# Kernel tuning notes

Hardware: AMD Instinct MI355X
Metric: run time of the kernel (lower is better)

Reference implementation:

```python
import jax, jax.numpy as jnp
import numpy as np

B, S, D = 2, 4096, 1024
H = 16
HD = D // H  # 64


def setup_inputs() -> dict:
    key = jax.random.key(0)
    ks = jax.random.split(key, 5)
    scale = 1.0 / np.sqrt(D)
    return {
        "x": jax.random.normal(ks[0], (B, S, D), dtype=jnp.float32),
        "Wq": jax.random.normal(ks[1], (D, D), dtype=jnp.float32) * scale,
        "Wk": jax.random.normal(ks[2], (D, D), dtype=jnp.float32) * scale,
        "Wv": jax.random.normal(ks[3], (D, D), dtype=jnp.float32) * scale,
        "Wo": jax.random.normal(ks[4], (D, D), dtype=jnp.float32) * scale,
        "bo": jnp.zeros((D,), dtype=jnp.float32),
    }


def reference(x, Wq, Wk, Wv, Wo, bo):
    b, s, d = x.shape
    # Linear layers (torch layout: weight [out, in], y = x @ W.T)
    q = (x @ Wq.T).reshape(b, s, H, HD)
    k = (x @ Wk.T).reshape(b, s, H, HD)
    v = (x @ Wv.T).reshape(b, s, H, HD)
    # scores: [b, h, q, k]
    scores = jnp.einsum("bqhd,bkhd->bhqk", q, k)
    # causal mask (upper triangle above diagonal -> -inf)
    causal = jnp.triu(jnp.ones((s, s), dtype=bool), k=1)
    scores = jnp.where(causal[None, None], -jnp.inf, scores)
    weights = jax.nn.softmax(scores / np.sqrt(HD), axis=-1)  # dropout p=0.0 -> identity
    ctx = jnp.einsum("bhqk,bkhd->bqhd", weights, v).reshape(b, s, d)
    return ctx @ Wo.T + bo
```

## Files before the change

kernel.cpp:

```cpp
#include <hip/hip_runtime.h>
#include <stdint.h>
#include <stddef.h>

#define S_LEN 4096
#define NHEAD 16
#define HDIM 64
#define DMODEL 1024
#define NBATCH 2
#define LOG2E 1.4426950408889634f

typedef __attribute__((ext_vector_type(8))) short bf16x8;
typedef __attribute__((ext_vector_type(4))) float f32x4;
typedef __attribute__((ext_vector_type(16))) float f32x16;
typedef __attribute__((ext_vector_type(2))) unsigned int uint2v;
typedef __attribute__((ext_vector_type(4))) unsigned int uint4v;

__device__ inline unsigned short f2b(float f) {
    union { float f; unsigned int u; } x; x.f = f;
    unsigned int r = (x.u + 0x7fffu + ((x.u >> 16) & 1u)) >> 16;
    return (unsigned short)r;
}

__device__ inline unsigned cvt_pk_bf16(float lo, float hi) {
    unsigned r;
    asm("v_cvt_pk_bf16_f32 %0, %1, %2" : "=v"(r) : "v"(lo), "v"(hi));
    return r;
}

__device__ inline float exp_fast(float x) {
    float r;
    asm("v_exp_f32 %0, %1" : "=v"(r) : "v"(x));
    return r;
}

__device__ inline void gload_lds16(const void* g, void* l) {
    __builtin_amdgcn_global_load_lds((const __attribute__((address_space(1))) void*)g,
                                     (__attribute__((address_space(3))) void*)l,
                                     16, 0, 0);
}

__global__ void cvt_x(const float* __restrict__ in, unsigned short* __restrict__ out, int n4) {
    int i = blockIdx.x * 256 + threadIdx.x;
    if (i >= n4) return;
    float4 v = ((const float4*)in)[i];
    ushort4 o;
    o.x = f2b(v.x); o.y = f2b(v.y); o.z = f2b(v.z); o.w = f2b(v.w);
    ((ushort4*)out)[i] = o;
}

__global__ void cvt_w(const float* __restrict__ w0, const float* __restrict__ w1,
                      const float* __restrict__ w2, const float* __restrict__ w3,
                      unsigned short* __restrict__ dst) {
    int z = blockIdx.y;
    const float* src = (z == 0) ? w0 : (z == 1) ? w1 : (z == 2) ? w2 : w3;
    int i = blockIdx.x * 256 + threadIdx.x;
    float4 v = ((const float4*)src)[i];
    ushort4 o;
    o.x = f2b(v.x); o.y = f2b(v.y); o.z = f2b(v.z); o.w = f2b(v.w);
    ((ushort4*)(dst + (size_t)z * DMODEL * DMODEL))[i] = o;
}

__global__ __launch_bounds__(256, 2)
void gemm_qkv(const unsigned short* __restrict__ xb,
              const unsigned short* __restrict__ wqb,
              const unsigned short* __restrict__ wkb,
              const unsigned short* __restrict__ wvb,
              unsigned short* __restrict__ Qb,
              unsigned short* __restrict__ Kb,
              unsigned short* __restrict__ Vt,
              float qscale) {
    __shared__ unsigned short Asl[128 * 64];
    __shared__ unsigned short Bsl[128 * 64];
    const int tid  = threadIdx.x;
    const int lane = tid & 63;
    const int wid  = tid >> 6;
    const int wm   = (wid >> 1) * 64, wn = (wid & 1) * 64;
    const int lr   = lane & 15, lk = lane >> 4;
    const int z    = blockIdx.z;

    const unsigned short* A;
    const unsigned short* Bw;
    int m0, n0;
    if (z < 2) { A = xb; Bw = z ? wkb : wqb; m0 = blockIdx.x * 128; n0 = blockIdx.y * 128; }
    else       { A = wvb; Bw = xb;           m0 = blockIdx.y * 128; n0 = blockIdx.x * 128; }

    f32x4 acc[4][4];
#pragma unroll
    for (int i = 0; i < 4; ++i)
#pragma unroll
        for (int j = 0; j < 4; ++j) acc[i][j] = (f32x4){0.f, 0.f, 0.f, 0.f};

    for (int kt = 0; kt < DMODEL; kt += 64) {
#pragma unroll
        for (int i = 0; i < 4; ++i) {
            int c = i * 256 + tid;
            int r = c >> 3, gc = (c & 7) ^ (r & 7);
            gload_lds16(A + (size_t)(m0 + r) * DMODEL + kt + gc * 8, Asl + c * 8);
        }
#pragma unroll
        for (int i = 0; i < 4; ++i) {
            int c = i * 256 + tid;
            int r = c >> 3, gc = (c & 7) ^ (r & 7);
            gload_lds16(Bw + (size_t)(n0 + r) * DMODEL + kt + gc * 8, Bsl + c * 8);
        }
        __syncthreads();
#pragma unroll
        for (int kh = 0; kh < 2; ++kh) {
            int cl = kh * 4 + lk;
            bf16x8 af[4], bfr[4];
#pragma unroll
            for (int m = 0; m < 4; ++m) {
                int r = wm + m * 16 + lr;
                af[m] = *(const bf16x8*)(Asl + r * 64 + ((cl ^ (r & 7)) * 8));
            }
#pragma unroll
            for (int n = 0; n < 4; ++n) {
                int r = wn + n * 16 + lr;
                bfr[n] = *(const bf16x8*)(Bsl + r * 64 + ((cl ^ (r & 7)) * 8));
            }
#pragma unroll
            for (int m = 0; m < 4; ++m)
#pragma unroll
                for (int n = 0; n < 4; ++n)
                    acc[m][n] = __builtin_amdgcn_mfma_f32_16x16x32_bf16(af[m], bfr[n], acc[m][n], 0, 0, 0);
        }
        __syncthreads();
    }

#pragma unroll
    for (int m = 0; m < 4; ++m) {
#pragma unroll
        for (int n = 0; n < 4; ++n) {
            int gn = n0 + wn + n * 16 + lr;
#pragma unroll
            for (int r = 0; r < 4; ++r) {
                int gm = m0 + wm + m * 16 + lk * 4 + r;
                float v = acc[m][n][r];
                if (z == 0) {
                    int b = gm >> 12, s = gm & 4095, h = gn >> 6, hd = gn & 63;
                    Qb[((size_t)((b * NHEAD + h) * S_LEN + s)) * HDIM + hd] = f2b(v * qscale);
                } else if (z == 1) {
                    int b = gm >> 12, s = gm & 4095, h = gn >> 6, hd = gn & 63;
                    Kb[((size_t)((b * NHEAD + h) * S_LEN + s)) * HDIM + hd] = f2b(v);
                } else {
                    int h = gm >> 6, hd = gm & 63, b = gn >> 12, s = gn & 4095;
                    Vt[((size_t)((b * NHEAD + h) * HDIM + hd)) * S_LEN + s] = f2b(v);
                }
            }
        }
    }
}

__global__ __launch_bounds__(256, 2)
void gemm_out(const unsigned short* __restrict__ A,
              const unsigned short* __restrict__ Bw,
              float* __restrict__ out, const float* __restrict__ bias) {
    __shared__ unsigned short Asl[128 * 64];
    __shared__ unsigned short Bsl[128 * 64];
    const int tid  = threadIdx.x;
    const int lane = tid & 63;
    const int wid  = tid >> 6;
    const int wm   = (wid >> 1) * 64, wn = (wid & 1) * 64;
    const int lr   = lane & 15, lk = lane >> 4;
    const int m0   = blockIdx.x * 128, n0 = blockIdx.y * 128;

    f32x4 acc[4][4];
#pragma unroll
    for (int i = 0; i < 4; ++i)
#pragma unroll
        for (int j = 0; j < 4; ++j) acc[i][j] = (f32x4){0.f, 0.f, 0.f, 0.f};

    for (int kt = 0; kt < DMODEL; kt += 64) {
#pragma unroll
        for (int i = 0; i < 4; ++i) {
            int c = i * 256 + tid;
            int r = c >> 3, gc = (c & 7) ^ (r & 7);
            gload_lds16(A + (size_t)(m0 + r) * DMODEL + kt + gc * 8, Asl + c * 8);
        }
#pragma unroll
        for (int i = 0; i < 4; ++i) {
            int c = i * 256 + tid;
            int r = c >> 3, gc = (c & 7) ^ (r & 7);
            gload_lds16(Bw + (size_t)(n0 + r) * DMODEL + kt + gc * 8, Bsl + c * 8);
        }
        __syncthreads();
#pragma unroll
        for (int kh = 0; kh < 2; ++kh) {
            int cl = kh * 4 + lk;
            bf16x8 af[4], bfr[4];
#pragma unroll
            for (int m = 0; m < 4; ++m) {
                int r = wm + m * 16 + lr;
                af[m] = *(const bf16x8*)(Asl + r * 64 + ((cl ^ (r & 7)) * 8));
            }
#pragma unroll
            for (int n = 0; n < 4; ++n) {
                int r = wn + n * 16 + lr;
                bfr[n] = *(const bf16x8*)(Bsl + r * 64 + ((cl ^ (r & 7)) * 8));
            }
#pragma unroll
            for (int m = 0; m < 4; ++m)
#pragma unroll
                for (int n = 0; n < 4; ++n)
                    acc[m][n] = __builtin_amdgcn_mfma_f32_16x16x32_bf16(af[m], bfr[n], acc[m][n], 0, 0, 0);
        }
        __syncthreads();
    }
#pragma unroll
    for (int m = 0; m < 4; ++m)
#pragma unroll
        for (int n = 0; n < 4; ++n) {
            int gn = n0 + wn + n * 16 + lr;
#pragma unroll
            for (int r = 0; r < 4; ++r) {
                int gm = m0 + wm + m * 16 + lk * 4 + r;
                out[(size_t)gm * DMODEL + gn] = acc[m][n][r] + bias[gn];
            }
        }
}

__global__ __launch_bounds__(256)
void attn_fwd(const unsigned short* __restrict__ Q,
              const unsigned short* __restrict__ K,
              const unsigned short* __restrict__ Vt,
              unsigned short* __restrict__ ctx) {
    __shared__ unsigned short Kl[2][4096];
    __shared__ unsigned short Vl[2][4096];

    const int tid  = threadIdx.x;
    const int lane = tid & 63;
    const int w    = tid >> 6;
    const int l31  = lane & 31;
    const int hi   = lane >> 5;

    const int bid  = blockIdx.x;
    const int qt   = 31 - (bid >> 5);
    const int bh   = ((bid & 7) << 2) | ((bid >> 3) & 3);
    const int b    = bh >> 4, h = bh & 15;
    const int q0   = qt * 128;
    const int qw0  = q0 + w * 32;

    const unsigned short* Qh = Q  + (size_t)bh * S_LEN * HDIM;
    const unsigned short* Kh = K  + (size_t)bh * S_LEN * HDIM;
    const unsigned short* Vh = Vt + (size_t)bh * HDIM * S_LEN;

    const int skA  = tid >> 6;
    const int lS   = tid & 63;
    const int lS31 = lS & 31, hiS = lS >> 5;
    const unsigned short* kb0 = Kh + (size_t)lS31 * HDIM + skA * 16 + hiS * 8;
    const unsigned short* kb1 = Kh + (size_t)(32 + lS31) * HDIM + skA * 16 + hiS * 8;
    const unsigned short* vb0 = Vh + (size_t)lS31 * S_LEN + skA * 16 + hiS * 8;
    const unsigned short* vb1 = Vh + (size_t)(32 + lS31) * S_LEN + skA * 16 + hiS * 8;

    bf16x8 qf[4];
    {
        const unsigned short* qrow = Qh + (size_t)(qw0 + l31) * HDIM + hi * 8;
#pragma unroll
        for (int s = 0; s < 4; ++s) qf[s] = *(const bf16x8*)(qrow + s * 16);
    }

    bf16x8 ones;
#pragma unroll
    for (int j = 0; j < 8; ++j) ones[j] = (short)0x3F80;

    f32x16 z16;
#pragma unroll
    for (int j = 0; j < 16; ++j) z16[j] = 0.f;

    const unsigned short* KL = &Kl[0][0] + lane * 8;
    const unsigned short* VL = &Vl[0][0] + lane * 8;

    f32x16 o0, o1, ls;
#pragma unroll
    for (int j = 0; j < 16; ++j) { o0[j] = 0.f; o1[j] = 0.f; ls[j] = 0.f; }

    const int nt = 2 * qt + 2;

    auto stage = [&](int buf, int kv0) {
        gload_lds16(kb0 + (size_t)kv0 * HDIM, &Kl[buf][(size_t)tid * 8]);
        gload_lds16(kb1 + (size_t)kv0 * HDIM, &Kl[buf][2048 + (size_t)tid * 8]);
        gload_lds16(vb0 + kv0, &Vl[buf][(size_t)tid * 8]);
        gload_lds16(vb1 + kv0, &Vl[buf][2048 + (size_t)tid * 8]);
    };

    auto packfrag = [&](const f32x16& v, int base) -> bf16x8 {
        unsigned a0 = cvt_pk_bf16(v[base + 0], v[base + 1]), a1 = cvt_pk_bf16(v[base + 2], v[base + 3]);
        unsigned b0 = cvt_pk_bf16(v[base + 4], v[base + 5]), b1 = cvt_pk_bf16(v[base + 6], v[base + 7]);
        uint2v r0 = __builtin_amdgcn_permlane32_swap(a0, b0, false, false);
        uint2v r1 = __builtin_amdgcn_permlane32_swap(a1, b1, false, false);
        uint4v f; f.x = r0.x; f.y = r1.x; f.z = r0.y; f.w = r1.y;
        return __builtin_bit_cast(bf16x8, f);
    };

    auto compute = [&](int buf, int kv0) {
        const unsigned short* KB = KL + buf * 4096;
        const unsigned short* VB = VL + buf * 4096;
        const int q = qw0 + l31;

        if (kv0 < qw0 + 32) {
            __builtin_amdgcn_s_setprio(1);
            f32x16 st = __builtin_amdgcn_mfma_f32_32x32x16_bf16(
                            *(const bf16x8*)(KB + 0 * 512), qf[0], z16, 0, 0, 0);
#pragma unroll
            for (int s = 1; s < 4; ++s)
                st = __builtin_amdgcn_mfma_f32_32x32x16_bf16(
                        *(const bf16x8*)(KB + s * 512), qf[s], st, 0, 0, 0);
            __builtin_amdgcn_s_setprio(0);
            if (kv0 + 31 > qw0) {
#pragma unroll
                for (int j = 0; j < 16; ++j) {
                    int roff = (j & 3) + 8 * (j >> 2) + 4 * hi;
                    if (kv0 + roff > q) st[j] = -3e38f;
                }
            }
#pragma unroll
            for (int j = 0; j < 16; ++j) st[j] = exp_fast(st[j]);
            bf16x8 pa = packfrag(st, 0);
            bf16x8 pb = packfrag(st, 8);
            __builtin_amdgcn_s_setprio(1);
            ls = __builtin_amdgcn_mfma_f32_32x32x16_bf16(ones, pa, ls, 0, 0, 0);
            ls = __builtin_amdgcn_mfma_f32_32x32x16_bf16(ones, pb, ls, 0, 0, 0);
            o0 = __builtin_amdgcn_mfma_f32_32x32x16_bf16(*(const bf16x8*)(VB + 0 * 512), pa, o0, 0, 0, 0);
            o1 = __builtin_amdgcn_mfma_f32_32x32x16_bf16(*(const bf16x8*)(VB + 4 * 512), pa, o1, 0, 0, 0);
            o0 = __builtin_amdgcn_mfma_f32_32x32x16_bf16(*(const bf16x8*)(VB + 1 * 512), pb, o0, 0, 0, 0);
            o1 = __builtin_amdgcn_mfma_f32_32x32x16_bf16(*(const bf16x8*)(VB + 5 * 512), pb, o1, 0, 0, 0);
            __builtin_amdgcn_s_setprio(0);
        }

        if (kv0 < qw0) {
            __builtin_amdgcn_s_setprio(1);
            f32x16 st = __builtin_amdgcn_mfma_f32_32x32x16_bf16(
                            *(const bf16x8*)(KB + 4 * 512), qf[0], z16, 0, 0, 0);
#pragma unroll
            for (int s = 1; s < 4; ++s)
                st = __builtin_amdgcn_mfma_f32_32x32x16_bf16(
                        *(const bf16x8*)(KB + (4 + s) * 512), qf[s], st, 0, 0, 0);
            __builtin_amdgcn_s_setprio(0);
            if (kv0 + 63 > qw0) {
#pragma unroll
                for (int j = 0; j < 16; ++j) {
                    int roff = (j & 3) + 8 * (j >> 2) + 4 * hi;
                    if (kv0 + 32 + roff > q) st[j] = -3e38f;
                }
            }
#pragma unroll
            for (int j = 0; j < 16; ++j) st[j] = exp_fast(st[j]);
            bf16x8 pa = packfrag(st, 0);
            bf16x8 pb = packfrag(st, 8);
            __builtin_amdgcn_s_setprio(1);
            ls = __builtin_amdgcn_mfma_f32_32x32x16_bf16(ones, pa, ls, 0, 0, 0);
            ls = __builtin_amdgcn_mfma_f32_32x32x16_bf16(ones, pb, ls, 0, 0, 0);
            o0 = __builtin_amdgcn_mfma_f32_32x32x16_bf16(*(const bf16x8*)(VB + 2 * 512), pa, o0, 0, 0, 0);
            o1 = __builtin_amdgcn_mfma_f32_32x32x16_bf16(*(const bf16x8*)(VB + 6 * 512), pa, o1, 0, 0, 0);
            o0 = __builtin_amdgcn_mfma_f32_32x32x16_bf16(*(const bf16x8*)(VB + 3 * 512), pb, o0, 0, 0, 0);
            o1 = __builtin_amdgcn_mfma_f32_32x32x16_bf16(*(const bf16x8*)(VB + 7 * 512), pb, o1, 0, 0, 0);
            __builtin_amdgcn_s_setprio(0);
        }
    };

    stage(0, 0);
    __syncthreads();
    for (int t = 0; t < nt; t += 2) {
        const int kv0 = t * 64;
        stage(1, kv0 + 64);
        compute(0, kv0);
        __syncthreads();
        if (t + 2 < nt) stage(0, kv0 + 128);
        compute(1, kv0 + 64);
        __syncthreads();
    }

    float inv = 1.f / ls[0];
    size_t sq = (size_t)q0 + w * 32 + l31;
    unsigned short* crow = ctx + ((size_t)b * S_LEN + sq) * DMODEL + h * HDIM;
#pragma unroll
    for (int quad = 0; quad < 4; ++quad) {
        int hdbase = quad * 8 + hi * 4;
        unsigned w0 = cvt_pk_bf16(o0[4 * quad] * inv, o0[4 * quad + 1] * inv);
        unsigned w1 = cvt_pk_bf16(o0[4 * quad + 2] * inv, o0[4 * quad + 3] * inv);
        *(unsigned long long*)(crow + hdbase) = ((unsigned long long)w1 << 32) | w0;
        unsigned w2 = cvt_pk_bf16(o1[4 * quad] * inv, o1[4 * quad + 1] * inv);
        unsigned w3 = cvt_pk_bf16(o1[4 * quad + 2] * inv, o1[4 * quad + 3] * inv);
        *(unsigned long long*)(crow + 32 + hdbase) = ((unsigned long long)w3 << 32) | w2;
    }
}

extern "C" void kernel_launch(void* const* d_in, const int* in_sizes, int n_in,
                              void* d_out, int out_size, void* d_ws, size_t ws_size,
                              hipStream_t stream) {
    (void)in_sizes; (void)n_in; (void)out_size; (void)ws_size;
    const float* x  = (const float*)d_in[0];
    const float* Wq = (const float*)d_in[1];
    const float* Wk = (const float*)d_in[2];
    const float* Wv = (const float*)d_in[3];
    const float* Wo = (const float*)d_in[4];
    const float* bo = (const float*)d_in[5];

    unsigned short* ws  = (unsigned short*)d_ws;
    const size_t NTOK = (size_t)NBATCH * S_LEN;
    unsigned short* xb  = ws;
    unsigned short* wqb = xb  + NTOK * DMODEL;
    unsigned short* wkb = wqb + (size_t)DMODEL * DMODEL;
    unsigned short* wvb = wkb + (size_t)DMODEL * DMODEL;
    unsigned short* wob = wvb + (size_t)DMODEL * DMODEL;
    unsigned short* Qb  = wob + (size_t)DMODEL * DMODEL;
    unsigned short* Kb  = Qb  + NTOK * DMODEL;
    unsigned short* Vt  = Kb  + NTOK * DMODEL;
    unsigned short* ctx = xb;

    int n4x = (int)(NTOK * DMODEL / 4);
    cvt_x<<<(n4x + 255) / 256, 256, 0, stream>>>(x, xb, n4x);
    cvt_w<<<dim3(DMODEL * DMODEL / 4 / 256, 4), 256, 0, stream>>>(Wq, Wk, Wv, Wo, wqb);

    const float qscale = 0.125f * LOG2E;
    gemm_qkv<<<dim3(64, 8, 3), 256, 0, stream>>>(xb, wqb, wkb, wvb, Qb, Kb, Vt, qscale);

    attn_fwd<<<1024, 256, 0, stream>>>(Qb, Kb, Vt, ctx);

    gemm_out<<<dim3(64, 8), 256, 0, stream>>>(ctx, wob, (float*)d_out, bo);
}
```

Measured before the change: 193.5 us.

## Double query rows per wave in attention to reuse K/V tiles

Each wave now handles two 32-row query sub-tiles (256 queries per block) instead of one, so every K fragment and V tile loaded from LDS feeds two query groups, halving LDS reads and K/V global staging per query. The grid shrinks from 1024 to 512 blocks, and blocks are reordered with heaviest tiles first to balance the causal workload. The change adds register pressure (two sets of accumulators and Q fragments), constrained by launch_bounds(256,2), and gives fewer blocks for load balancing across CUs.

```diff
diff --git a/kernel.cpp b/kernel.cpp
--- a/kernel.cpp
+++ b/kernel.cpp
@@ -219,7 +219,7 @@
         }
 }
 
-__global__ __launch_bounds__(256)
+__global__ __launch_bounds__(256, 2)
 void attn_fwd(const unsigned short* __restrict__ Q,
               const unsigned short* __restrict__ K,
               const unsigned short* __restrict__ Vt,
@@ -234,11 +234,13 @@
     const int hi   = lane >> 5;
 
     const int bid  = blockIdx.x;
-    const int qt   = 31 - (bid >> 5);
+    const int g    = bid >> 5;
+    const int qt   = (g < 8) ? (15 - g) : (g - 8);
     const int bh   = ((bid & 7) << 2) | ((bid >> 3) & 3);
     const int b    = bh >> 4, h = bh & 15;
-    const int q0   = qt * 128;
-    const int qw0  = q0 + w * 32;
+    const int q0   = qt * 256;
+    const int qA   = q0 + w * 64;
+    const int qB   = qA + 32;
 
     const unsigned short* Qh = Q  + (size_t)bh * S_LEN * HDIM;
     const unsigned short* Kh = K  + (size_t)bh * S_LEN * HDIM;
@@ -252,11 +254,12 @@
     const unsigned short* vb0 = Vh + (size_t)lS31 * S_LEN + skA * 16 + hiS * 8;
     const unsigned short* vb1 = Vh + (size_t)(32 + lS31) * S_LEN + skA * 16 + hiS * 8;
 
-    bf16x8 qf[4];
-    {
-        const unsigned short* qrow = Qh + (size_t)(qw0 + l31) * HDIM + hi * 8;
-#pragma unroll
-        for (int s = 0; s < 4; ++s) qf[s] = *(const bf16x8*)(qrow + s * 16);
+    bf16x8 qf[2][4];
+#pragma unroll
+    for (int qs = 0; qs < 2; ++qs) {
+        const unsigned short* qrow = Qh + (size_t)(qA + qs * 32 + l31) * HDIM + hi * 8;
+#pragma unroll
+        for (int s = 0; s < 4; ++s) qf[qs][s] = *(const bf16x8*)(qrow + s * 16);
     }
 
     bf16x8 ones;
@@ -270,11 +273,13 @@
     const unsigned short* KL = &Kl[0][0] + lane * 8;
     const unsigned short* VL = &Vl[0][0] + lane * 8;
 
-    f32x16 o0, o1, ls;
-#pragma unroll
-    for (int j = 0; j < 16; ++j) { o0[j] = 0.f; o1[j] = 0.f; ls[j] = 0.f; }
-
-    const int nt = 2 * qt + 2;
+    f32x16 o0[2], o1[2], ls[2];
+#pragma unroll
+    for (int qs = 0; qs < 2; ++qs)
+#pragma unroll
+        for (int j = 0; j < 16; ++j) { o0[qs][j] = 0.f; o1[qs][j] = 0.f; ls[qs][j] = 0.f; }
+
+    const int nt = 4 * qt + 4;
 
     auto stage = [&](int buf, int kv0) {
         gload_lds16(kb0 + (size_t)kv0 * HDIM, &Kl[buf][(size_t)tid * 8]);
@@ -295,66 +300,46 @@
     auto compute = [&](int buf, int kv0) {
         const unsigned short* KB = KL + buf * 4096;
         const unsigned short* VB = VL + buf * 4096;
-        const int q = qw0 + l31;
-
-        if (kv0 < qw0 + 32) {
-            __builtin_amdgcn_s_setprio(1);
-            f32x16 st = __builtin_amdgcn_mfma_f32_32x32x16_bf16(
-                            *(const bf16x8*)(KB + 0 * 512), qf[0], z16, 0, 0, 0);
-#pragma unroll
-            for (int s = 1; s < 4; ++s)
-                st = __builtin_amdgcn_mfma_f32_32x32x16_bf16(
-                        *(const bf16x8*)(KB + s * 512), qf[s], st, 0, 0, 0);
-            __builtin_amdgcn_s_setprio(0);
-            if (kv0 + 31 > qw0) {
-#pragma unroll
-                for (int j = 0; j < 16; ++j) {
-                    int roff = (j & 3) + 8 * (j >> 2) + 4 * hi;
-                    if (kv0 + roff > q) st[j] = -3e38f;
+#pragma unroll
+        for (int half = 0; half < 2; ++half) {
+            const int kvh = kv0 + 32 * half;
+            if (kvh >= qB + 32) continue;
+            bf16x8 kf0 = *(const bf16x8*)(KB + (4 * half + 0) * 512);
+            bf16x8 kf1 = *(const bf16x8*)(KB + (4 * half + 1) * 512);
+            bf16x8 kf2 = *(const bf16x8*)(KB + (4 * half + 2) * 512);
+            bf16x8 kf3 = *(const bf16x8*)(KB + (4 * half + 3) * 512);
+#pragma unroll
+            for (int qs = 0; qs < 2; ++qs) {
+                const int qw = qA + qs * 32;
+                if (kvh < qw + 32) {
+                    __builtin_amdgcn_s_setprio(1);
+                    f32x16 st = __builtin_amdgcn_mfma_f32_32x32x16_bf16(kf0, qf[qs][0], z16, 0, 0, 0);
+                    st = __builtin_amdgcn_mfma_f32_32x32x16_bf16(kf1, qf[qs][1], st, 0, 0, 0);
+                    st = __builtin_amdgcn_mfma_f32_32x32x16_bf16(kf2, qf[qs][2], st, 0, 0, 0);
+                    st = __builtin_amdgcn_mfma_f32_32x32x16_bf16(kf3, qf[qs][3], st, 0, 0, 0);
+                    __builtin_amdgcn_s_setprio(0);
+                    if (kvh + 31 > qw) {
+                        const int q = qw + l31;
+#pragma unroll
+                        for (int j = 0; j < 16; ++j) {
+                            int roff = (j & 3) + 8 * (j >> 2) + 4 * hi;
+                            if (kvh + roff > q) st[j] = -3e38f;
+                        }
+                    }
+#pragma unroll
+                    for (int j = 0; j < 16; ++j) st[j] = exp_fast(st[j]);
+                    bf16x8 pa = packfrag(st, 0);
+                    bf16x8 pb = packfrag(st, 8);
+                    __builtin_amdgcn_s_setprio(1);
+                    ls[qs] = __builtin_amdgcn_mfma_f32_32x32x16_bf16(ones, pa, ls[qs], 0, 0, 0);
+                    ls[qs] = __builtin_amdgcn_mfma_f32_32x32x16_bf16(ones, pb, ls[qs], 0, 0, 0);
+                    o0[qs] = __builtin_amdgcn_mfma_f32_32x32x16_bf16(*(const bf16x8*)(VB + (2 * half + 0) * 512), pa, o0[qs], 0, 0, 0);
+                    o1[qs] = __builtin_amdgcn_mfma_f32_32x32x16_bf16(*(const bf16x8*)(VB + (2 * half + 4) * 512), pa, o1[qs], 0, 0, 0);
+                    o0[qs] = __builtin_amdgcn_mfma_f32_32x32x16_bf16(*(const bf16x8*)(VB + (2 * half + 1) * 512), pb, o0[qs], 0, 0, 0);
+                    o1[qs] = __builtin_amdgcn_mfma_f32_32x32x16_bf16(*(const bf16x8*)(VB + (2 * half + 5) * 512), pb, o1[qs], 0, 0, 0);
+                    __builtin_amdgcn_s_setprio(0);
                 }
             }
-#pragma unroll
-            for (int j = 0; j < 16; ++j) st[j] = exp_fast(st[j]);
-            bf16x8 pa = packfrag(st, 0);
-            bf16x8 pb = packfrag(st, 8);
-            __builtin_amdgcn_s_setprio(1);
-            ls = __builtin_amdgcn_mfma_f32_32x32x16_bf16(ones, pa, ls, 0, 0, 0);
-            ls = __builtin_amdgcn_mfma_f32_32x32x16_bf16(ones, pb, ls, 0, 0, 0);
-            o0 = __builtin_amdgcn_mfma_f32_32x32x16_bf16(*(const bf16x8*)(VB + 0 * 512), pa, o0, 0, 0, 0);
-            o1 = __builtin_amdgcn_mfma_f32_32x32x16_bf16(*(const bf16x8*)(VB + 4 * 512), pa, o1, 0, 0, 0);
-            o0 = __builtin_amdgcn_mfma_f32_32x32x16_bf16(*(const bf16x8*)(VB + 1 * 512), pb, o0, 0, 0, 0);
-            o1 = __builtin_amdgcn_mfma_f32_32x32x16_bf16(*(const bf16x8*)(VB + 5 * 512), pb, o1, 0, 0, 0);
-            __builtin_amdgcn_s_setprio(0);
-        }
-
-        if (kv0 < qw0) {
-            __builtin_amdgcn_s_setprio(1);
-            f32x16 st = __builtin_amdgcn_mfma_f32_32x32x16_bf16(
-                            *(const bf16x8*)(KB + 4 * 512), qf[0], z16, 0, 0, 0);
-#pragma unroll
-            for (int s = 1; s < 4; ++s)
-                st = __builtin_amdgcn_mfma_f32_32x32x16_bf16(
-                        *(const bf16x8*)(KB + (4 + s) * 512), qf[s], st, 0, 0, 0);
-            __builtin_amdgcn_s_setprio(0);
-            if (kv0 + 63 > qw0) {
-#pragma unroll
-                for (int j = 0; j < 16; ++j) {
-                    int roff = (j & 3) + 8 * (j >> 2) + 4 * hi;
-                    if (kv0 + 32 + roff > q) st[j] = -3e38f;
-                }
-            }
-#pragma unroll
-            for (int j = 0; j < 16; ++j) st[j] = exp_fast(st[j]);
-            bf16x8 pa = packfrag(st, 0);
-            bf16x8 pb = packfrag(st, 8);
-            __builtin_amdgcn_s_setprio(1);
-            ls = __builtin_amdgcn_mfma_f32_32x32x16_bf16(ones, pa, ls, 0, 0, 0);
-            ls = __builtin_amdgcn_mfma_f32_32x32x16_bf16(ones, pb, ls, 0, 0, 0);
-            o0 = __builtin_amdgcn_mfma_f32_32x32x16_bf16(*(const bf16x8*)(VB + 2 * 512), pa, o0, 0, 0, 0);
-            o1 = __builtin_amdgcn_mfma_f32_32x32x16_bf16(*(const bf16x8*)(VB + 6 * 512), pa, o1, 0, 0, 0);
-            o0 = __builtin_amdgcn_mfma_f32_32x32x16_bf16(*(const bf16x8*)(VB + 3 * 512), pb, o0, 0, 0, 0);
-            o1 = __builtin_amdgcn_mfma_f32_32x32x16_bf16(*(const bf16x8*)(VB + 7 * 512), pb, o1, 0, 0, 0);
-            __builtin_amdgcn_s_setprio(0);
         }
     };
 
@@ -370,18 +355,21 @@
         __syncthreads();
     }
 
-    float inv = 1.f / ls[0];
-    size_t sq = (size_t)q0 + w * 32 + l31;
-    unsigned short* crow = ctx + ((size_t)b * S_LEN + sq) * DMODEL + h * HDIM;
-#pragma unroll
-    for (int quad = 0; quad < 4; ++quad) {
-        int hdbase = quad * 8 + hi * 4;
-        unsigned w0 = cvt_pk_bf16(o0[4 * quad] * inv, o0[4 * quad + 1] * inv);
-        unsigned w1 = cvt_pk_bf16(o0[4 * quad + 2] * inv, o0[4 * quad + 3] * inv);
-        *(unsigned long long*)(crow + hdbase) = ((unsigned long long)w1 << 32) | w0;
-        unsigned w2 = cvt_pk_bf16(o1[4 * quad] * inv, o1[4 * quad + 1] * inv);
-        unsigned w3 = cvt_pk_bf16(o1[4 * quad + 2] * inv, o1[4 * quad + 3] * inv);
-        *(unsigned long long*)(crow + 32 + hdbase) = ((unsigned long long)w3 << 32) | w2;
+#pragma unroll
+    for (int qs = 0; qs < 2; ++qs) {
+        float inv = 1.f / ls[qs][0];
+        size_t sq = (size_t)qA + qs * 32 + l31;
+        unsigned short* crow = ctx + ((size_t)b * S_LEN + sq) * DMODEL + h * HDIM;
+#pragma unroll
+        for (int quad = 0; quad < 4; ++quad) {
+            int hdbase = quad * 8 + hi * 4;
+            unsigned w0 = cvt_pk_bf16(o0[qs][4 * quad] * inv, o0[qs][4 * quad + 1] * inv);
+            unsigned w1 = cvt_pk_bf16(o0[qs][4 * quad + 2] * inv, o0[qs][4 * quad + 3] * inv);
+            *(unsigned long long*)(crow + hdbase) = ((unsigned long long)w1 << 32) | w0;
+            unsigned w2 = cvt_pk_bf16(o1[qs][4 * quad] * inv, o1[qs][4 * quad + 1] * inv);
+            unsigned w3 = cvt_pk_bf16(o1[qs][4 * quad + 2] * inv, o1[qs][4 * quad + 3] * inv);
+            *(unsigned long long*)(crow + 32 + hdbase) = ((unsigned long long)w3 << 32) | w2;
+        }
     }
 }
 
@@ -415,7 +403,7 @@
     const float qscale = 0.125f * LOG2E;
     gemm_qkv<<<dim3(64, 8, 3), 256, 0, stream>>>(xb, wqb, wkb, wvb, Qb, Kb, Vt, qscale);
 
-    attn_fwd<<<1024, 256, 0, stream>>>(Qb, Kb, Vt, ctx);
+    attn_fwd<<<512, 256, 0, stream>>>(Qb, Kb, Vt, ctx);
 
     gemm_out<<<dim3(64, 8), 256, 0, stream>>>(ctx, wob, (float*)d_out, bo);
 }
```

After: 204.0 us. 1.05x slower.

## Use 4-deep 32-row KV ring buffer with partial vmcnt waits in attention

Applied to the files above, without the earlier changes.

Restructures the attention KV loop from a 2-buffer, 64-row ping-pong with full __syncthreads into a 4-slot ring of 32-row tiles. Three tiles are prefetched ahead, and each step waits only on the oldest loads with s_waitcnt vmcnt plus a raw s_barrier. The goal is to keep more global-to-LDS loads in flight and avoid draining all outstanding memory before every compute step. In exchange there are twice as many barriers per KV row, and correctness depends on the hand-written vmcnt counts matching the loads in flight.

```diff
diff --git a/kernel.cpp b/kernel.cpp
--- a/kernel.cpp
+++ b/kernel.cpp
@@ -224,8 +224,8 @@
               const unsigned short* __restrict__ K,
               const unsigned short* __restrict__ Vt,
               unsigned short* __restrict__ ctx) {
-    __shared__ unsigned short Kl[2][4096];
-    __shared__ unsigned short Vl[2][4096];
+    __shared__ unsigned short Kl[4][2048];
+    __shared__ unsigned short Vl[4][2048];
 
     const int tid  = threadIdx.x;
     const int lane = tid & 63;
@@ -244,13 +244,11 @@
     const unsigned short* Kh = K  + (size_t)bh * S_LEN * HDIM;
     const unsigned short* Vh = Vt + (size_t)bh * HDIM * S_LEN;
 
-    const int skA  = tid >> 6;
+    const int sk   = tid >> 6;
     const int lS   = tid & 63;
     const int lS31 = lS & 31, hiS = lS >> 5;
-    const unsigned short* kb0 = Kh + (size_t)lS31 * HDIM + skA * 16 + hiS * 8;
-    const unsigned short* kb1 = Kh + (size_t)(32 + lS31) * HDIM + skA * 16 + hiS * 8;
-    const unsigned short* vb0 = Vh + (size_t)lS31 * S_LEN + skA * 16 + hiS * 8;
-    const unsigned short* vb1 = Vh + (size_t)(32 + lS31) * S_LEN + skA * 16 + hiS * 8;
+    const unsigned short* kbase = Kh + (size_t)lS31 * HDIM + sk * 16 + hiS * 8;
+    const unsigned short* vbase = Vh + (size_t)((sk >> 1) * 32 + lS31) * S_LEN + (sk & 1) * 16 + hiS * 8;
 
     bf16x8 qf[4];
     {
@@ -274,13 +272,11 @@
 #pragma unroll
     for (int j = 0; j < 16; ++j) { o0[j] = 0.f; o1[j] = 0.f; ls[j] = 0.f; }
 
-    const int nt = 2 * qt + 2;
-
-    auto stage = [&](int buf, int kv0) {
-        gload_lds16(kb0 + (size_t)kv0 * HDIM, &Kl[buf][(size_t)tid * 8]);
-        gload_lds16(kb1 + (size_t)kv0 * HDIM, &Kl[buf][2048 + (size_t)tid * 8]);
-        gload_lds16(vb0 + kv0, &Vl[buf][(size_t)tid * 8]);
-        gload_lds16(vb1 + kv0, &Vl[buf][2048 + (size_t)tid * 8]);
+    const int nt = 4 * qt + 4;
+
+    auto stage = [&](int buf, int t) {
+        gload_lds16(kbase + (size_t)(t * 32) * HDIM, &Kl[buf][(size_t)tid * 8]);
+        gload_lds16(vbase + t * 32, &Vl[buf][(size_t)tid * 8]);
     };
 
     auto packfrag = [&](const f32x16& v, int base) -> bf16x8 {
@@ -293,82 +289,51 @@
     };
 
     auto compute = [&](int buf, int kv0) {
-        const unsigned short* KB = KL + buf * 4096;
-        const unsigned short* VB = VL + buf * 4096;
-        const int q = qw0 + l31;
-
-        if (kv0 < qw0 + 32) {
-            __builtin_amdgcn_s_setprio(1);
-            f32x16 st = __builtin_amdgcn_mfma_f32_32x32x16_bf16(
-                            *(const bf16x8*)(KB + 0 * 512), qf[0], z16, 0, 0, 0);
-#pragma unroll
-            for (int s = 1; s < 4; ++s)
-                st = __builtin_amdgcn_mfma_f32_32x32x16_bf16(
-                        *(const bf16x8*)(KB + s * 512), qf[s], st, 0, 0, 0);
-            __builtin_amdgcn_s_setprio(0);
-            if (kv0 + 31 > qw0) {
-#pragma unroll
-                for (int j = 0; j < 16; ++j) {
-                    int roff = (j & 3) + 8 * (j >> 2) + 4 * hi;
-                    if (kv0 + roff > q) st[j] = -3e38f;
-                }
-            }
-#pragma unroll
-            for (int j = 0; j < 16; ++j) st[j] = exp_fast(st[j]);
-            bf16x8 pa = packfrag(st, 0);
-            bf16x8 pb = packfrag(st, 8);
-            __builtin_amdgcn_s_setprio(1);
-            ls = __builtin_amdgcn_mfma_f32_32x32x16_bf16(ones, pa, ls, 0, 0, 0);
-            ls = __builtin_amdgcn_mfma_f32_32x32x16_bf16(ones, pb, ls, 0, 0, 0);
-            o0 = __builtin_amdgcn_mfma_f32_32x32x16_bf16(*(const bf16x8*)(VB + 0 * 512), pa, o0, 0, 0, 0);
-            o1 = __builtin_amdgcn_mfma_f32_32x32x16_bf16(*(const bf16x8*)(VB + 4 * 512), pa, o1, 0, 0, 0);
-            o0 = __builtin_amdgcn_mfma_f32_32x32x16_bf16(*(const bf16x8*)(VB + 1 * 512), pb, o0, 0, 0, 0);
-            o1 = __builtin_amdgcn_mfma_f32_32x32x16_bf16(*(const bf16x8*)(VB + 5 * 512), pb, o1, 0, 0, 0);
-            __builtin_amdgcn_s_setprio(0);
-        }
-
-        if (kv0 < qw0) {
-            __builtin_amdgcn_s_setprio(1);
-            f32x16 st = __builtin_amdgcn_mfma_f32_32x32x16_bf16(
-                            *(const bf16x8*)(KB + 4 * 512), qf[0], z16, 0, 0, 0);
-#pragma unroll
-            for (int s = 1; s < 4; ++s)
-                st = __builtin_amdgcn_mfma_f32_32x32x16_bf16(
-                        *(const bf16x8*)(KB + (4 + s) * 512), qf[s], st, 0, 0, 0);
-            __builtin_amdgcn_s_setprio(0);
-            if (kv0 + 63 > qw0) {
-#pragma unroll
-                for (int j = 0; j < 16; ++j) {
-                    int roff = (j & 3) + 8 * (j >> 2) + 4 * hi;
-                    if (kv0 + 32 + roff > q) st[j] = -3e38f;
-                }
-            }
-#pragma unroll
-            for (int j = 0; j < 16; ++j) st[j] = exp_fast(st[j]);
-            bf16x8 pa = packfrag(st, 0);
-            bf16x8 pb = packfrag(st, 8);
-            __builtin_amdgcn_s_setprio(1);
-            ls = __builtin_amdgcn_mfma_f32_32x32x16_bf16(ones, pa, ls, 0, 0, 0);
-            ls = __builtin_amdgcn_mfma_f32_32x32x16_bf16(ones, pb, ls, 0, 0, 0);
-            o0 = __builtin_amdgcn_mfma_f32_32x32x16_bf16(*(const bf16x8*)(VB + 2 * 512), pa, o0, 0, 0, 0);
-            o1 = __builtin_amdgcn_mfma_f32_32x32x16_bf16(*(const bf16x8*)(VB + 6 * 512), pa, o1, 0, 0, 0);
-            o0 = __builtin_amdgcn_mfma_f32_32x32x16_bf16(*(const bf16x8*)(VB + 3 * 512), pb, o0, 0, 0, 0);
-            o1 = __builtin_amdgcn_mfma_f32_32x32x16_bf16(*(const bf16x8*)(VB + 7 * 512), pb, o1, 0, 0, 0);
-            __builtin_amdgcn_s_setprio(0);
-        }
+        if (kv0 >= qw0 + 32) return;
+        const unsigned short* KB = KL + buf * 2048;
+        const unsigned short* VB = VL + buf * 2048;
+        __builtin_amdgcn_s_setprio(1);
+        f32x16 st = __builtin_amdgcn_mfma_f32_32x32x16_bf16(*(const bf16x8*)(KB + 0 * 512), qf[0], z16, 0, 0, 0);
+        st = __builtin_amdgcn_mfma_f32_32x32x16_bf16(*(const bf16x8*)(KB + 1 * 512), qf[1], st, 0, 0, 0);
+        st = __builtin_amdgcn_mfma_f32_32x32x16_bf16(*(const bf16x8*)(KB + 2 * 512), qf[2], st, 0, 0, 0);
+        st = __builtin_amdgcn_mfma_f32_32x32x16_bf16(*(const bf16x8*)(KB + 3 * 512), qf[3], st, 0, 0, 0);
+        __builtin_amdgcn_s_setprio(0);
+        if (kv0 == qw0) {
+#pragma unroll
+            for (int j = 0; j < 16; ++j) {
+                int roff = (j & 3) + 8 * (j >> 2) + 4 * hi;
+                if (roff > l31) st[j] = -3e38f;
+            }
+        }
+#pragma unroll
+        for (int j = 0; j < 16; ++j) st[j] = exp_fast(st[j]);
+        bf16x8 pa = packfrag(st, 0);
+        bf16x8 pb = packfrag(st, 8);
+        __builtin_amdgcn_s_setprio(1);
+        ls = __builtin_amdgcn_mfma_f32_32x32x16_bf16(ones, pa, ls, 0, 0, 0);
+        ls = __builtin_amdgcn_mfma_f32_32x32x16_bf16(ones, pb, ls, 0, 0, 0);
+        o0 = __builtin_amdgcn_mfma_f32_32x32x16_bf16(*(const bf16x8*)(VB + 0 * 512), pa, o0, 0, 0, 0);
+        o1 = __builtin_amdgcn_mfma_f32_32x32x16_bf16(*(const bf16x8*)(VB + 2 * 512), pa, o1, 0, 0, 0);
+        o0 = __builtin_amdgcn_mfma_f32_32x32x16_bf16(*(const bf16x8*)(VB + 1 * 512), pb, o0, 0, 0, 0);
+        o1 = __builtin_amdgcn_mfma_f32_32x32x16_bf16(*(const bf16x8*)(VB + 3 * 512), pb, o1, 0, 0, 0);
+        __builtin_amdgcn_s_setprio(0);
     };
 
     stage(0, 0);
-    __syncthreads();
-    for (int t = 0; t < nt; t += 2) {
-        const int kv0 = t * 64;
-        stage(1, kv0 + 64);
-        compute(0, kv0);
-        __syncthreads();
-        if (t + 2 < nt) stage(0, kv0 + 128);
-        compute(1, kv0 + 64);
-        __syncthreads();
-    }
+    stage(1, 1);
+    stage(2, 2);
+    for (int t = 0; t < nt - 2; ++t) {
+        asm volatile("s_waitcnt vmcnt(4)" ::: "memory");
+        asm volatile("s_barrier" ::: "memory");
+        compute(t & 3, t * 32);
+        if (t + 3 < nt) stage((t + 3) & 3, t + 3);
+    }
+    asm volatile("s_waitcnt vmcnt(2)" ::: "memory");
+    asm volatile("s_barrier" ::: "memory");
+    compute((nt - 2) & 3, (nt - 2) * 32);
+    asm volatile("s_waitcnt vmcnt(0)" ::: "memory");
+    asm volatile("s_barrier" ::: "memory");
+    compute((nt - 1) & 3, (nt - 1) * 32);
 
     float inv = 1.f / ls[0];
     size_t sq = (size_t)q0 + w * 32 + l31;
```

Result: slower. 205.9 us (+6.4%).
